# Kernel optimization log

Measured on AMD Instinct MI355X. Metric: run time of the kernel, lower is better.

The kernel has to match this reference:

```python
import jax, jax.numpy as jnp
import numpy as np

EMBD_DIM = 1024
HEAD_SIZE = 64


def setup_inputs() -> dict:
    key = jax.random.key(0)
    kx, kq, kk, kv = jax.random.split(key, 4)
    x = jax.random.normal(kx, (4, 4096, EMBD_DIM), dtype=jnp.float32)
    # nn.Linear(embd_dim, head_size, bias=False) weights, stored as [C, H] so x @ W
    s = 1.0 / np.sqrt(EMBD_DIM)
    Wq = jax.random.uniform(kq, (EMBD_DIM, HEAD_SIZE), jnp.float32, -s, s)
    Wk = jax.random.uniform(kk, (EMBD_DIM, HEAD_SIZE), jnp.float32, -s, s)
    Wv = jax.random.uniform(kv, (EMBD_DIM, HEAD_SIZE), jnp.float32, -s, s)
    return {"x": x, "Wq": Wq, "Wk": Wk, "Wv": Wv}


def reference(x, Wq, Wk, Wv):
    # q,k,v: [B, T, H]
    q = jnp.einsum("btc,ch->bth", x, Wq)
    k = jnp.einsum("btc,ch->bth", x, Wk)
    v = jnp.einsum("btc,ch->bth", x, Wv)
    scale = k.shape[-1] ** -0.5
    # full [B, T, T] score matrix, as in the original naive implementation
    scores = jnp.einsum("bth,bsh->bts", q, k) * scale
    attn = jax.nn.softmax(scores, axis=-1)
    # dropout p=0.0 -> identity
    out = jnp.einsum("bts,bsh->bth", attn, v)  # [B, T, H]
    return out
```

## Files before the change

### kernel.cpp

```cpp
#include <hip/hip_runtime.h>
#include <hip/hip_bf16.h>

#define B_ 4
#define T_ 4096
#define C_ 1024
#define H_ 64

typedef float  f32x4  __attribute__((ext_vector_type(4)));
typedef short  bf16x8 __attribute__((ext_vector_type(8)));
typedef uint   u32x4  __attribute__((ext_vector_type(4)));

static __device__ __forceinline__ ushort f2bf(float f) {
  union { float f; uint u; } v; v.f = f;
  uint u = v.u;
  u += 0x7FFFu + ((u >> 16) & 1u);
  return (ushort)(u >> 16);
}

static __device__ __forceinline__ uint cvtpk(float s0, float s1) {
  uint r;
  asm("v_cvt_pk_bf16_f32 %0, %1, %2" : "=v"(r) : "v"(s0), "v"(s1));
  return r;
}

static __device__ __forceinline__ void gload_lds16(const void* g, void* l) {
  __builtin_amdgcn_global_load_lds(
      (const __attribute__((address_space(1))) unsigned int*)g,
      (__attribute__((address_space(3))) unsigned int*)l, 16, 0, 0);
}

#define MFMA(a, b, c) __builtin_amdgcn_mfma_f32_16x16x32_bf16(a, b, c, 0, 0, 0)

__global__ __launch_bounds__(256) void wt_prep(const float* __restrict__ Wq,
                                               const float* __restrict__ Wk,
                                               const float* __restrict__ Wv,
                                               ushort* __restrict__ WtF) {
  int idx = blockIdx.x * 256 + threadIdx.x;
  int w = idx >> 16, idx2 = idx & 65535;
  int c = idx2 >> 6, n = idx2 & 63;
  const float* W = (w == 0) ? Wq : (w == 1) ? Wk : Wv;
  float v = W[idx2];
  int c64 = c >> 6, kc = (c >> 5) & 1, g = (c >> 3) & 3, j = c & 7;
  int nt = n >> 4, l15 = n & 15;
  size_t dst = ((size_t)((((w * 16 + c64) * 2 + kc) * 4 + nt) * 64 + g * 16 + l15)) * 8 + j;
  WtF[dst] = f2bf(v);
}

__global__ __launch_bounds__(256) void qkv_proj(const float* __restrict__ x,
                                                const ushort* __restrict__ WtF,
                                                ushort* __restrict__ Qg,
                                                char* __restrict__ KaF,
                                                char* __restrict__ VaF) {
  __shared__ __align__(16) ushort wl[2][12288];
  const int tid = threadIdx.x;
  const int lane = tid & 63, wid = tid >> 6;
  const int l15 = lane & 15, g = lane >> 4;
  const int b = blockIdx.x >> 6, rt = blockIdx.x & 63;
  const int wrow = rt * 64 + wid * 16;

  f32x4 acc[3][4];
  #pragma unroll
  for (int w = 0; w < 3; w++)
    #pragma unroll
    for (int nt = 0; nt < 4; nt++) acc[w][nt] = (f32x4)0.0f;

  const float* xr = x + ((size_t)b * T_ + wrow + l15) * C_ + g * 8;

  auto stagew = [&](int buf, int c64) {
    char* dst = (char*)wl[buf] + tid * 16;
    const char* src = (const char*)WtF + (size_t)c64 * 8192 + tid * 16;
    #pragma unroll
    for (int p = 0; p < 6; p++)
      gload_lds16(src + (p >> 1) * 131072 + (p & 1) * 4096, dst + p * 4096);
  };

  f32x4 xp[3][4];
  auto xload = [&](int slot, int t) {
    const float* src = xr + t * 64;
    xp[slot][0] = *(const f32x4*)src;
    xp[slot][1] = *(const f32x4*)(src + 4);
    xp[slot][2] = *(const f32x4*)(src + 32);
    xp[slot][3] = *(const f32x4*)(src + 36);
  };

  stagew(0, 0);
  xload(0, 0);
  xload(1, 1);
  asm volatile("s_waitcnt vmcnt(8)" ::: "memory");
  __builtin_amdgcn_s_barrier();
  __builtin_amdgcn_sched_barrier(0);

  #pragma unroll
  for (int t = 0; t < 16; t++) {
    const int cur = t & 1;
    if (t < 15) stagew(cur ^ 1, t + 1);
    if (t < 14) xload((t + 2) % 3, t + 2);

    const int slot = t % 3;
    bf16x8 xa[2];
    #pragma unroll
    for (int kc = 0; kc < 2; kc++) {
      union { uint u[4]; bf16x8 v; } h;
      f32x4 c0 = xp[slot][2 * kc], c1 = xp[slot][2 * kc + 1];
      h.u[0] = cvtpk(c0[0], c0[1]); h.u[1] = cvtpk(c0[2], c0[3]);
      h.u[2] = cvtpk(c1[0], c1[1]); h.u[3] = cvtpk(c1[2], c1[3]);
      xa[kc] = h.v;
    }
    const char* wb = (const char*)wl[cur] + lane * 16;
    __builtin_amdgcn_s_setprio(1);
    #pragma unroll
    for (int w = 0; w < 3; w++)
      #pragma unroll
      for (int kc = 0; kc < 2; kc++)
        #pragma unroll
        for (int nt = 0; nt < 4; nt++) {
          bf16x8 wf = *(const bf16x8*)(wb + w * 8192 + kc * 4096 + nt * 1024);
          acc[w][nt] = MFMA(xa[kc], wf, acc[w][nt]);
        }
    __builtin_amdgcn_s_setprio(0);

    if (t < 15) {
      if (t < 14) asm volatile("s_waitcnt vmcnt(4)" ::: "memory");
      else        asm volatile("s_waitcnt vmcnt(0)" ::: "memory");
      __builtin_amdgcn_s_barrier();
      __builtin_amdgcn_sched_barrier(0);
    }
  }

  char* kdst = KaF + ((size_t)b * 64 + rt) * 8192;
  char* vdst = VaF + ((size_t)b * 128 + (wrow >> 5)) * 4096;
  #pragma unroll
  for (int nt = 0; nt < 4; nt++) {
    int n = nt * 16 + l15;
    int kc = n >> 5, gp2 = (n >> 3) & 3, j2 = n & 7;
    #pragma unroll
    for (int r = 0; r < 4; r++) {
      int tt = wrow + g * 4 + r;
      Qg[((size_t)b * T_ + tt) * H_ + n] = f2bf(acc[0][nt][r]);
      int key = tt & 63;
      *(ushort*)(kdst + kc * 4096 + (key >> 4) * 1024 +
                 (gp2 * 16 + (key & 15)) * 16 + j2 * 2) = f2bf(acc[1][nt][r]);
      int k5 = tt & 31;
      int gp = ((k5 >> 4) << 1) | ((k5 >> 2) & 1);
      int js = ((k5 >> 3) & 1) * 4 + (k5 & 3);
      *(ushort*)(vdst + nt * 1024 + (gp * 16 + l15) * 16 + js * 2) = f2bf(acc[2][nt][r]);
    }
  }
}

__global__ __launch_bounds__(256, 2) void attn(const ushort* __restrict__ Qg,
                                               const char* __restrict__ KaF,
                                               const char* __restrict__ VaF,
                                               ushort* __restrict__ Op,
                                               float* __restrict__ Ds,
                                               float* __restrict__ out,
                                               int KT) {
  __shared__ __align__(16) char kv[3][16384];
  const int tid = threadIdx.x;
  const int lane = tid & 63, wid = tid >> 6;
  const int bid = blockIdx.x;
  const int b = bid & 3;
  const int qt = (bid >> 2) & 31, s = bid >> 7;
  const int l15 = lane & 15, g = lane >> 4;

  bf16x8 qa[2][2];
  #pragma unroll
  for (int qs = 0; qs < 2; qs++) {
    const ushort* qp = Qg + ((size_t)b * T_ + qt * 128 + wid * 32 + qs * 16 + l15) * H_ + g * 8;
    qa[qs][0] = *(const bf16x8*)qp;
    qa[qs][1] = *(const bf16x8*)(qp + 32);
  }

  f32x4 oacc[2][4];
  #pragma unroll
  for (int qs = 0; qs < 2; qs++)
    #pragma unroll
    for (int nt = 0; nt < 4; nt++) oacc[qs][nt] = (f32x4)0.0f;
  float dsum[2] = {0.f, 0.f};

  const char* kbase = KaF + (size_t)b * 64 * 8192;
  const char* vbase = VaF + (size_t)b * 128 * 4096;
  const int it0 = s * KT;

  auto stage = [&](int buf, int it) {
    char* dst = kv[buf] + tid * 16;
    const char* ks = kbase + (size_t)it * 8192 + tid * 16;
    const char* vs = vbase + (size_t)it * 8192 + tid * 16;
    gload_lds16(ks, dst);
    gload_lds16(ks + 4096, dst + 4096);
    gload_lds16(vs, dst + 8192);
    gload_lds16(vs + 4096, dst + 12288);
  };

  stage(0, it0);
  stage(1, it0 + 1);
  asm volatile("s_waitcnt vmcnt(4)" ::: "memory");
  __builtin_amdgcn_s_barrier();
  __builtin_amdgcn_sched_barrier(0);

  int cur = 0;
  for (int it = 0; it < KT; it++) {
    int pf = cur + 2; if (pf >= 3) pf -= 3;
    if (it + 2 < KT) stage(pf, it0 + it + 2);
    const char* kl = kv[cur];
    const char* vl = kv[cur] + 8192;

    f32x4 sacc[2][4];
    #pragma unroll
    for (int qs = 0; qs < 2; qs++)
      #pragma unroll
      for (int nt = 0; nt < 4; nt++) sacc[qs][nt] = (f32x4)0.0f;
    __builtin_amdgcn_s_setprio(1);
    #pragma unroll
    for (int nt = 0; nt < 4; nt++)
      #pragma unroll
      for (int kc = 0; kc < 2; kc++) {
        bf16x8 ka = *(const bf16x8*)(kl + kc * 4096 + nt * 1024 + lane * 16);
        sacc[0][nt] = MFMA(ka, qa[0][kc], sacc[0][nt]);
        sacc[1][nt] = MFMA(ka, qa[1][kc], sacc[1][nt]);
      }
    __builtin_amdgcn_s_setprio(0);

    uint t0[2][4], t1[2][4];
    #pragma unroll
    for (int qs = 0; qs < 2; qs++)
      #pragma unroll
      for (int nt = 0; nt < 4; nt++) {
        float p0 = __builtin_amdgcn_exp2f(sacc[qs][nt][0] * 0.18033688011112042f);
        float p1 = __builtin_amdgcn_exp2f(sacc[qs][nt][1] * 0.18033688011112042f);
        float p2 = __builtin_amdgcn_exp2f(sacc[qs][nt][2] * 0.18033688011112042f);
        float p3 = __builtin_amdgcn_exp2f(sacc[qs][nt][3] * 0.18033688011112042f);
        dsum[qs] += (p0 + p1) + (p2 + p3);
        t0[qs][nt] = cvtpk(p0, p1);
        t1[qs][nt] = cvtpk(p2, p3);
      }

    #pragma unroll
    for (int kk = 0; kk < 2; kk++) {
      bf16x8 pf2[2];
      #pragma unroll
      for (int qs = 0; qs < 2; qs++) {
        uint x0 = t0[qs][2 * kk], y0 = t0[qs][2 * kk + 1];
        uint x1 = t1[qs][2 * kk], y1 = t1[qs][2 * kk + 1];
        asm volatile("v_permlane32_swap_b32 %0, %1" : "+v"(x0), "+v"(y0));
        asm volatile("v_permlane32_swap_b32 %0, %1" : "+v"(x1), "+v"(y1));
        union { uint u[4]; bf16x8 v; } pfu;
        pfu.u[0] = x0; pfu.u[1] = x1; pfu.u[2] = y0; pfu.u[3] = y1;
        pf2[qs] = pfu.v;
      }
      __builtin_amdgcn_s_setprio(1);
      #pragma unroll
      for (int ntd = 0; ntd < 4; ntd++) {
        bf16x8 va = *(const bf16x8*)(vl + kk * 4096 + ntd * 1024 + lane * 16);
        oacc[0][ntd] = MFMA(va, pf2[0], oacc[0][ntd]);
        oacc[1][ntd] = MFMA(va, pf2[1], oacc[1][ntd]);
      }
      __builtin_amdgcn_s_setprio(0);
    }

    if (it + 1 < KT) {
      if (it + 2 < KT) asm volatile("s_waitcnt vmcnt(4)" ::: "memory");
      else             asm volatile("s_waitcnt vmcnt(0)" ::: "memory");
      __builtin_amdgcn_s_barrier();
      __builtin_amdgcn_sched_barrier(0);
    }
    cur = cur + 1; if (cur >= 3) cur -= 3;
  }

  #pragma unroll
  for (int qs = 0; qs < 2; qs++) {
    float d = dsum[qs];
    d += __shfl_xor(d, 16, 64);
    d += __shfl_xor(d, 32, 64);
    const int q = qt * 128 + wid * 32 + qs * 16 + l15;
    if (Op != nullptr) {
      ushort* ob = Op + ((size_t)(s * 4 + b) * T_ + q) * H_;
      #pragma unroll
      for (int nt = 0; nt < 4; nt++) {
        uint2 pk;
        pk.x = cvtpk(oacc[qs][nt][0], oacc[qs][nt][1]);
        pk.y = cvtpk(oacc[qs][nt][2], oacc[qs][nt][3]);
        *(uint2*)(ob + nt * 16 + g * 4) = pk;
      }
      if (g == 0) Ds[(size_t)(s * 4 + b) * T_ + q] = d;
    } else {
      float inv = 1.0f / d;
      float* ob = out + ((size_t)b * T_ + q) * H_;
      #pragma unroll
      for (int nt = 0; nt < 4; nt++)
        #pragma unroll
        for (int r = 0; r < 4; r++) ob[nt * 16 + g * 4 + r] = oacc[qs][nt][r] * inv;
    }
  }
}

__global__ __launch_bounds__(256) void reduce_seg(const ushort* __restrict__ Op,
                                                  const float* __restrict__ Ds,
                                                  float* __restrict__ out, int seg) {
  int i = blockIdx.x * 256 + threadIdx.x;
  size_t e = (size_t)i * 4;
  int row = (int)(e >> 6);
  f32x4 o = (f32x4)0.0f;
  float d = 0.0f;
  for (int s = 0; s < seg; s++) {
    uint2 pk = *(const uint2*)(Op + (size_t)s * ((size_t)B_ * T_ * H_) + e);
    union { uint u; float f; } c0, c1, c2, c3;
    c0.u = (pk.x & 0xFFFFu) << 16; c1.u = (pk.x >> 16) << 16;
    c2.u = (pk.y & 0xFFFFu) << 16; c3.u = (pk.y >> 16) << 16;
    o[0] += c0.f; o[1] += c1.f; o[2] += c2.f; o[3] += c3.f;
    d += Ds[(size_t)s * ((size_t)B_ * T_) + row];
  }
  *(f32x4*)(out + e) = o * (1.0f / d);
}

extern "C" void kernel_launch(void* const* d_in, const int* in_sizes, int n_in,
                              void* d_out, int out_size, void* d_ws, size_t ws_size,
                              hipStream_t stream) {
  const float* x  = (const float*)d_in[0];
  const float* Wq = (const float*)d_in[1];
  const float* Wk = (const float*)d_in[2];
  const float* Wv = (const float*)d_in[3];
  float* out = (float*)d_out;

  char* ws = (char*)d_ws;
  size_t off = 0;
  auto take = [&](size_t n) -> void* {
    void* p = ws + off;
    off = (off + n + 255) & ~(size_t)255;
    return p;
  };
  ushort* Qg  = (ushort*)take((size_t)B_ * T_ * H_ * 2);
  char*   KaF = (char*)take((size_t)B_ * T_ * H_ * 2);
  char*   VaF = (char*)take((size_t)B_ * T_ * H_ * 2);
  ushort* WtF = (ushort*)take((size_t)3 * H_ * C_ * 2);

  int seg = 1;
  ushort* Op = nullptr;
  float* Ds = nullptr;
  for (int sg = 4; sg >= 2; sg >>= 1) {
    size_t need = off + (size_t)sg * B_ * T_ * H_ * 2 + 256 + (size_t)sg * B_ * T_ * 4 + 256;
    if (need <= ws_size) {
      seg = sg;
      Op = (ushort*)take((size_t)sg * B_ * T_ * H_ * 2);
      Ds = (float*)take((size_t)sg * B_ * T_ * 4);
      break;
    }
  }
  int KT = 64 / seg;

  wt_prep<<<768, 256, 0, stream>>>(Wq, Wk, Wv, WtF);
  qkv_proj<<<B_ * 64, 256, 0, stream>>>(x, WtF, Qg, KaF, VaF);
  attn<<<B_ * (T_ / 128) * seg, 256, 0, stream>>>(Qg, KaF, VaF, Op, Ds, out, KT);
  if (Op) reduce_seg<<<(B_ * T_ * H_ / 4 + 255) / 256, 256, 0, stream>>>(Op, Ds, out, seg);
}
```

Measured before the change: 55.60 us.

## Fold softmax scale into Wq and compute row sums with MFMA

Pre-multiplies Wq by the combined scale-times-log2e constant, so the attention loop no longer multiplies each score before exp2. The softmax denominator is now accumulated by an extra MFMA against a vector of bf16 ones instead of scalar adds plus cross-lane shuffles, which moves VALU work onto the matrix unit. It also interleaves exp and pack with the PV MFMAs per kk chunk and drops the min-2-blocks launch bound. The risks are that the denominator is now summed from bf16-rounded probabilities, and that register pressure or occupancy may change.

```diff
diff --git a/kernel.cpp b/kernel.cpp
--- a/kernel.cpp
+++ b/kernel.cpp
@@ -40,6 +40,7 @@
   int c = idx2 >> 6, n = idx2 & 63;
   const float* W = (w == 0) ? Wq : (w == 1) ? Wk : Wv;
   float v = W[idx2];
+  if (w == 0) v *= 0.18033688011112042f;
   int c64 = c >> 6, kc = (c >> 5) & 1, g = (c >> 3) & 3, j = c & 7;
   int nt = n >> 4, l15 = n & 15;
   size_t dst = ((size_t)((((w * 16 + c64) * 2 + kc) * 4 + nt) * 64 + g * 16 + l15)) * 8 + j;
@@ -148,13 +149,13 @@
   }
 }
 
-__global__ __launch_bounds__(256, 2) void attn(const ushort* __restrict__ Qg,
-                                               const char* __restrict__ KaF,
-                                               const char* __restrict__ VaF,
-                                               ushort* __restrict__ Op,
-                                               float* __restrict__ Ds,
-                                               float* __restrict__ out,
-                                               int KT) {
+__global__ __launch_bounds__(256) void attn(const ushort* __restrict__ Qg,
+                                            const char* __restrict__ KaF,
+                                            const char* __restrict__ VaF,
+                                            ushort* __restrict__ Op,
+                                            float* __restrict__ Ds,
+                                            float* __restrict__ out,
+                                            int KT) {
   __shared__ __align__(16) char kv[3][16384];
   const int tid = threadIdx.x;
   const int lane = tid & 63, wid = tid >> 6;
@@ -171,12 +172,19 @@
     qa[qs][1] = *(const bf16x8*)(qp + 32);
   }
 
+  union { ushort u[8]; bf16x8 v; } ones_u;
+  #pragma unroll
+  for (int i = 0; i < 8; i++) ones_u.u[i] = 0x3F80;
+  const bf16x8 ones = ones_u.v;
+
   f32x4 oacc[2][4];
-  #pragma unroll
-  for (int qs = 0; qs < 2; qs++)
+  f32x4 dacc[2];
+  #pragma unroll
+  for (int qs = 0; qs < 2; qs++) {
     #pragma unroll
     for (int nt = 0; nt < 4; nt++) oacc[qs][nt] = (f32x4)0.0f;
-  float dsum[2] = {0.f, 0.f};
+    dacc[qs] = (f32x4)0.0f;
+  }
 
   const char* kbase = KaF + (size_t)b * 64 * 8192;
   const char* vbase = VaF + (size_t)b * 128 * 4096;
@@ -200,8 +208,8 @@
 
   int cur = 0;
   for (int it = 0; it < KT; it++) {
-    int pf = cur + 2; if (pf >= 3) pf -= 3;
-    if (it + 2 < KT) stage(pf, it0 + it + 2);
+    int pfb = cur + 2; if (pfb >= 3) pfb -= 3;
+    if (it + 2 < KT) stage(pfb, it0 + it + 2);
     const char* kl = kv[cur];
     const char* vl = kv[cur] + 8192;
 
@@ -221,27 +229,16 @@
       }
     __builtin_amdgcn_s_setprio(0);
 
-    uint t0[2][4], t1[2][4];
-    #pragma unroll
-    for (int qs = 0; qs < 2; qs++)
-      #pragma unroll
-      for (int nt = 0; nt < 4; nt++) {
-        float p0 = __builtin_amdgcn_exp2f(sacc[qs][nt][0] * 0.18033688011112042f);
-        float p1 = __builtin_amdgcn_exp2f(sacc[qs][nt][1] * 0.18033688011112042f);
-        float p2 = __builtin_amdgcn_exp2f(sacc[qs][nt][2] * 0.18033688011112042f);
-        float p3 = __builtin_amdgcn_exp2f(sacc[qs][nt][3] * 0.18033688011112042f);
-        dsum[qs] += (p0 + p1) + (p2 + p3);
-        t0[qs][nt] = cvtpk(p0, p1);
-        t1[qs][nt] = cvtpk(p2, p3);
-      }
-
     #pragma unroll
     for (int kk = 0; kk < 2; kk++) {
       bf16x8 pf2[2];
       #pragma unroll
       for (int qs = 0; qs < 2; qs++) {
-        uint x0 = t0[qs][2 * kk], y0 = t0[qs][2 * kk + 1];
-        uint x1 = t1[qs][2 * kk], y1 = t1[qs][2 * kk + 1];
+        f32x4 sa = sacc[qs][2 * kk], sb = sacc[qs][2 * kk + 1];
+        uint x0 = cvtpk(__builtin_amdgcn_exp2f(sa[0]), __builtin_amdgcn_exp2f(sa[1]));
+        uint x1 = cvtpk(__builtin_amdgcn_exp2f(sa[2]), __builtin_amdgcn_exp2f(sa[3]));
+        uint y0 = cvtpk(__builtin_amdgcn_exp2f(sb[0]), __builtin_amdgcn_exp2f(sb[1]));
+        uint y1 = cvtpk(__builtin_amdgcn_exp2f(sb[2]), __builtin_amdgcn_exp2f(sb[3]));
         asm volatile("v_permlane32_swap_b32 %0, %1" : "+v"(x0), "+v"(y0));
         asm volatile("v_permlane32_swap_b32 %0, %1" : "+v"(x1), "+v"(y1));
         union { uint u[4]; bf16x8 v; } pfu;
@@ -255,6 +252,8 @@
         oacc[0][ntd] = MFMA(va, pf2[0], oacc[0][ntd]);
         oacc[1][ntd] = MFMA(va, pf2[1], oacc[1][ntd]);
       }
+      dacc[0] = MFMA(ones, pf2[0], dacc[0]);
+      dacc[1] = MFMA(ones, pf2[1], dacc[1]);
       __builtin_amdgcn_s_setprio(0);
     }
 
@@ -269,9 +268,7 @@
 
   #pragma unroll
   for (int qs = 0; qs < 2; qs++) {
-    float d = dsum[qs];
-    d += __shfl_xor(d, 16, 64);
-    d += __shfl_xor(d, 32, 64);
+    float d = dacc[qs][0];
     const int q = qt * 128 + wid * 32 + qs * 16 + l15;
     if (Op != nullptr) {
       ushort* ob = Op + ((size_t)(s * 4 + b) * T_ + q) * H_;
```

Measured after the change: 53.74 us. 1.03x faster.
